# Kernel tuning notes

Measured on AMD Instinct MI355X. Metric: run time of the kernel, lower is better.

## Reference

```python
import jax, jax.numpy as jnp
import numpy as np

B, D, L = 64, 1024, 2048  # batch, init dim, source length; context feature dim = D//2


def setup_inputs() -> dict:
    key = jax.random.key(0)
    k1, k2, k3, k4 = jax.random.split(key, 4)
    inp = jax.random.normal(k1, (B, D), dtype=jnp.float32)
    context = jax.random.normal(k2, (B, L, D // 2), dtype=jnp.float32)
    # torch Linear weights: [out_features, in_features]
    W_in = jax.random.normal(k3, (D, D), dtype=jnp.float32) * (1.0 / np.sqrt(D))
    W_out = jax.random.normal(k4, (D, 2 * D), dtype=jnp.float32) * (1.0 / np.sqrt(2 * D))
    return {"input": inp, "context": context, "W_in": W_in, "W_out": W_out}


def reference(input, context, W_in, W_out):
    Bv, Dv = input.shape
    # linear_in(input).view(B, D//2, 2): two query vectors of size D//2 per batch
    targetT = (input @ W_in.T).reshape(Bv, Dv // 2, 2)           # [B, D/2, 2]
    attn = jnp.einsum('bld,bdk->bkl', context, targetT)          # [B, 2, L]
    attn = jax.nn.softmax(attn, axis=-1)                         # softmax over sourceL
    weighted = jnp.einsum('bkl,bld->bkd', attn, context)         # [B, 2, D/2]
    weightedContext = weighted.reshape(Bv, Dv)                   # [B, D]
    combined = jnp.concatenate([weightedContext, input], axis=1) # [B, 2D]
    contextOutput = jnp.tanh(combined @ W_out.T)                 # [B, D]
    return contextOutput, attn[:, 0, :], attn[:, 1, :]
```

## Files before the change

kernel.cpp:

```cpp
#include <hip/hip_runtime.h>
#include <cmath>

#define NB 64
#define ND 1024
#define DH 512
#define NL 2048
#define NCHUNK 16
#define RPB 128
#define RPW 32
#define REC 520

__global__ __launch_bounds__(256) void k_gemm(const float* __restrict__ A,
                                              const float* __restrict__ W,
                                              float* __restrict__ out,
                                              int K, int do_tanh) {
  __shared__ float As[64][65];
  __shared__ float Ws[4][65];
  const int t = threadIdx.x;
  const int jt = blockIdx.x * 4;
  const int b = t & 63, jl = t >> 6;
  float acc = 0.f;
  for (int m0 = 0; m0 < K; m0 += 64) {
#pragma unroll
    for (int i = 0; i < 4; i++) {
      int f = t + i * 256;
      int r = f >> 4, c = (f & 15) * 4;
      const float4 v = *(const float4*)(A + (size_t)r * K + m0 + c);
      As[r][c] = v.x; As[r][c + 1] = v.y; As[r][c + 2] = v.z; As[r][c + 3] = v.w;
    }
    if (t < 64) {
      int r = t >> 4, c = (t & 15) * 4;
      const float4 v = *(const float4*)(W + (size_t)(jt + r) * K + m0 + c);
      Ws[r][c] = v.x; Ws[r][c + 1] = v.y; Ws[r][c + 2] = v.z; Ws[r][c + 3] = v.w;
    }
    __syncthreads();
#pragma unroll
    for (int mm = 0; mm < 64; mm++) acc += As[b][mm] * Ws[jl][mm];
    __syncthreads();
  }
  out[(size_t)b * ND + jt + jl] = do_tanh ? tanhf(acc) : acc;
}

__global__ __launch_bounds__(256, 4) void k2_attn(const float* __restrict__ ctx,
                                                  const float* __restrict__ tgt,
                                                  float* __restrict__ sc0,
                                                  float* __restrict__ sc1,
                                                  float* __restrict__ part) {
  const int chunk = blockIdx.x, b = blockIdx.y;
  const int wave = threadIdx.x >> 6, lane = threadIdx.x & 63;
  const float* crow = ctx + ((size_t)b * NL + chunk * RPB + wave * RPW) * DH + lane * 8;

  float t0[8], t1[8];
  {
    const float* tp = tgt + b * ND + lane * 16;
#pragma unroll
    for (int j = 0; j < 4; j++) {
      float4 v = *(const float4*)(tp + j * 4);
      t0[2 * j] = v.x; t1[2 * j] = v.y; t0[2 * j + 1] = v.z; t1[2 * j + 1] = v.w;
    }
  }

  float m0 = -INFINITY, l0 = 0.f, m1 = -INFINITY, l1 = 0.f;
  float a0[8], a1[8];
#pragma unroll
  for (int j = 0; j < 8; j++) { a0[j] = 0.f; a1[j] = 0.f; }
  float sv0 = 0.f, sv1 = 0.f;

  float4 pa = *(const float4*)(crow);
  float4 pb = *(const float4*)(crow + 4);
#pragma unroll 2
  for (int i = 0; i < RPW; i++) {
    float c[8] = {pa.x, pa.y, pa.z, pa.w, pb.x, pb.y, pb.z, pb.w};
    if (i + 1 < RPW) {
      pa = *(const float4*)(crow + (size_t)(i + 1) * DH);
      pb = *(const float4*)(crow + (size_t)(i + 1) * DH + 4);
    }
    float s0 = 0.f, s1 = 0.f;
#pragma unroll
    for (int j = 0; j < 8; j++) { s0 += c[j] * t0[j]; s1 += c[j] * t1[j]; }
#pragma unroll
    for (int off = 32; off > 0; off >>= 1) {
      s0 += __shfl_xor(s0, off);
      s1 += __shfl_xor(s1, off);
    }
    if (lane == i) { sv0 = s0; sv1 = s1; }
    if (s0 > m0) {
      float al = __expf(m0 - s0);
      m0 = s0; l0 *= al;
#pragma unroll
      for (int j = 0; j < 8; j++) a0[j] *= al;
    }
    {
      float p = __expf(s0 - m0);
      l0 += p;
#pragma unroll
      for (int j = 0; j < 8; j++) a0[j] += p * c[j];
    }
    if (s1 > m1) {
      float al = __expf(m1 - s1);
      m1 = s1; l1 *= al;
#pragma unroll
      for (int j = 0; j < 8; j++) a1[j] *= al;
    }
    {
      float p = __expf(s1 - m1);
      l1 += p;
#pragma unroll
      for (int j = 0; j < 8; j++) a1[j] += p * c[j];
    }
  }

  const int rowbase = b * NL + chunk * RPB + wave * RPW;
  if (lane < RPW) { sc0[rowbase + lane] = sv0; sc1[rowbase + lane] = sv1; }

  __shared__ float accS[4][1024];
  __shared__ float mlS[4][4];
#pragma unroll
  for (int j = 0; j < 8; j++) {
    accS[wave][lane * 8 + j] = a0[j];
    accS[wave][512 + lane * 8 + j] = a1[j];
  }
  if (lane == 0) { mlS[wave][0] = m0; mlS[wave][1] = l0; mlS[wave][2] = m1; mlS[wave][3] = l1; }
  __syncthreads();

  const int t = threadIdx.x;
  const int k = (t * 4) >> 9;
  const int d = (t * 4) & 511;
  float M = fmaxf(fmaxf(mlS[0][2 * k], mlS[1][2 * k]), fmaxf(mlS[2][2 * k], mlS[3][2 * k]));
  float Lk = 0.f;
  float v0 = 0.f, v1 = 0.f, v2 = 0.f, v3 = 0.f;
#pragma unroll
  for (int w = 0; w < 4; w++) {
    float e = __expf(mlS[w][2 * k] - M);
    Lk += mlS[w][2 * k + 1] * e;
    const float* ap = &accS[w][k * 512 + d];
    v0 += ap[0] * e; v1 += ap[1] * e; v2 += ap[2] * e; v3 += ap[3] * e;
  }
  float* rec = part + ((size_t)(b * NCHUNK + chunk) * 2 + k) * REC;
  if ((t & 127) == 0) { rec[0] = M; rec[1] = Lk; }
  rec[4 + d] = v0; rec[5 + d] = v1; rec[6 + d] = v2; rec[7 + d] = v3;
}

__global__ __launch_bounds__(256) void k3_combine(const float* __restrict__ part,
                                                  const float* __restrict__ inp,
                                                  float* __restrict__ combined,
                                                  float* __restrict__ sc0,
                                                  float* __restrict__ sc1) {
  const int b = blockIdx.x;
  const int t = threadIdx.x;
  __shared__ float MM[2], LL[2];
  if (t < 2) {
    const int k = t;
    float Mk = -INFINITY;
    for (int c = 0; c < NCHUNK; c++)
      Mk = fmaxf(Mk, part[((size_t)(b * NCHUNK + c) * 2 + k) * REC]);
    float Lk = 0.f;
    for (int c = 0; c < NCHUNK; c++) {
      const float* rec = part + ((size_t)(b * NCHUNK + c) * 2 + k) * REC;
      Lk += rec[1] * __expf(rec[0] - Mk);
    }
    MM[k] = Mk; LL[k] = Lk;
  }
  __syncthreads();

  const int k = (t * 4) >> 9, d = (t * 4) & 511;
  float v0 = 0.f, v1 = 0.f, v2 = 0.f, v3 = 0.f;
  for (int c = 0; c < NCHUNK; c++) {
    const float* rec = part + ((size_t)(b * NCHUNK + c) * 2 + k) * REC;
    float e = __expf(rec[0] - MM[k]);
    v0 += rec[4 + d] * e; v1 += rec[5 + d] * e; v2 += rec[6 + d] * e; v3 += rec[7 + d] * e;
  }
  const float inv = 1.f / LL[k];
  float* cp = combined + (size_t)b * 2048 + k * 512 + d;
  cp[0] = v0 * inv; cp[1] = v1 * inv; cp[2] = v2 * inv; cp[3] = v3 * inv;

  const float4 iv = *(const float4*)(inp + (size_t)b * ND + t * 4);
  *(float4*)(combined + (size_t)b * 2048 + 1024 + t * 4) = iv;

  const float M0 = MM[0], i0 = 1.f / LL[0];
  const float M1 = MM[1], i1 = 1.f / LL[1];
#pragma unroll
  for (int r = 0; r < 8; r++) {
    const int idx = b * NL + t * 8 + r;
    sc0[idx] = __expf(sc0[idx] - M0) * i0;
    sc1[idx] = __expf(sc1[idx] - M1) * i1;
  }
}

extern "C" void kernel_launch(void* const* d_in, const int* in_sizes, int n_in,
                              void* d_out, int out_size, void* d_ws, size_t ws_size,
                              hipStream_t stream) {
  const float* input   = (const float*)d_in[0];
  const float* context = (const float*)d_in[1];
  const float* W_in    = (const float*)d_in[2];
  const float* W_out   = (const float*)d_in[3];

  float* out   = (float*)d_out;
  float* attn0 = out + NB * ND;
  float* attn1 = attn0 + NB * NL;

  float* ws       = (float*)d_ws;
  float* target   = ws;
  float* combined = ws + NB * ND;
  float* part     = ws + NB * ND + NB * 2048;

  k_gemm<<<dim3(ND / 4), dim3(256), 0, stream>>>(input, W_in, target, ND, 0);
  k2_attn<<<dim3(NCHUNK, NB), dim3(256), 0, stream>>>(context, target, attn0, attn1, part);
  k3_combine<<<dim3(NB), dim3(256), 0, stream>>>(part, input, combined, attn0, attn1);
  k_gemm<<<dim3(ND / 4), dim3(256), 0, stream>>>(combined, W_out, out, 2 * ND, 1);
}
```

Measured before the change: 451.5 us.

## Split-K GEMMs with register-tiled weights and two-row batched online softmax

Both GEMMs are restructured into split-K kernels. Each wave computes 8 output columns for all 64 batch rows, reading weights directly from global memory as float4 and staging only the activation slab in shared memory; a separate reduce kernel sums the 8 partials and applies tanh where needed. The attention kernel now handles two context rows per iteration, so the online-softmax rescale and exp run once per row pair with a deeper register prefetch. The cost is two extra launches and a partial-sum buffer in workspace, traded against better weight reuse and less serial dependency in the softmax loop.

```diff
diff --git a/kernel.cpp b/kernel.cpp
--- a/kernel.cpp
+++ b/kernel.cpp
@@ -9,36 +9,66 @@
 #define RPB 128
 #define RPW 32
 #define REC 520
-
+#define KS 8
+
+template <int KK>
 __global__ __launch_bounds__(256) void k_gemm(const float* __restrict__ A,
                                               const float* __restrict__ W,
-                                              float* __restrict__ out,
-                                              int K, int do_tanh) {
-  __shared__ float As[64][65];
-  __shared__ float Ws[4][65];
+                                              float* __restrict__ part) {
+  constexpr int SLAB = KK / KS;
+  __shared__ float As[64][36];
   const int t = threadIdx.x;
-  const int jt = blockIdx.x * 4;
-  const int b = t & 63, jl = t >> 6;
-  float acc = 0.f;
-  for (int m0 = 0; m0 < K; m0 += 64) {
-#pragma unroll
-    for (int i = 0; i < 4; i++) {
-      int f = t + i * 256;
-      int r = f >> 4, c = (f & 15) * 4;
-      const float4 v = *(const float4*)(A + (size_t)r * K + m0 + c);
-      As[r][c] = v.x; As[r][c + 1] = v.y; As[r][c + 2] = v.z; As[r][c + 3] = v.w;
-    }
-    if (t < 64) {
-      int r = t >> 4, c = (t & 15) * 4;
-      const float4 v = *(const float4*)(W + (size_t)(jt + r) * K + m0 + c);
-      Ws[r][c] = v.x; Ws[r][c + 1] = v.y; Ws[r][c + 2] = v.z; Ws[r][c + 3] = v.w;
-    }
+  const int lane = t & 63;
+  const int wv = t >> 6;
+  const int k0 = blockIdx.y * SLAB;
+  const int j0 = __builtin_amdgcn_readfirstlane((int)(blockIdx.x * 32 + wv * 8));
+  const float* Wb = W + (size_t)j0 * KK + k0;
+
+  float acc[8];
+#pragma unroll
+  for (int j = 0; j < 8; j++) acc[j] = 0.f;
+
+  const int srow = t >> 2, sko = (t & 3) * 8;
+  const float* sbase = A + (size_t)srow * KK + k0 + sko;
+
+  for (int kc = 0; kc < SLAB; kc += 32) {
+    float4 v0 = *(const float4*)(sbase + kc);
+    float4 v1 = *(const float4*)(sbase + kc + 4);
     __syncthreads();
-#pragma unroll
-    for (int mm = 0; mm < 64; mm++) acc += As[b][mm] * Ws[jl][mm];
+    *(float4*)&As[srow][sko]     = v0;
+    *(float4*)&As[srow][sko + 4] = v1;
     __syncthreads();
-  }
-  out[(size_t)b * ND + jt + jl] = do_tanh ? tanhf(acc) : acc;
+#pragma unroll
+    for (int kk = 0; kk < 32; kk += 4) {
+      float4 av = *(const float4*)&As[lane][kk];
+      const float* wp = Wb + kc + kk;
+#pragma unroll
+      for (int j = 0; j < 8; j++) {
+        float4 wq = *(const float4*)(wp + (size_t)j * KK);
+        acc[j] = fmaf(av.x, wq.x, acc[j]);
+        acc[j] = fmaf(av.y, wq.y, acc[j]);
+        acc[j] = fmaf(av.z, wq.z, acc[j]);
+        acc[j] = fmaf(av.w, wq.w, acc[j]);
+      }
+    }
+  }
+  float* p = part + ((size_t)blockIdx.y * 64 + lane) * ND + j0;
+#pragma unroll
+  for (int j = 0; j < 8; j++) p[j] = acc[j];
+}
+
+template <int ACT>
+__global__ __launch_bounds__(256) void k_reduce(const float* __restrict__ part,
+                                                float* __restrict__ out) {
+  const int i = (blockIdx.x * 256 + threadIdx.x) * 4;
+  float4 s = make_float4(0.f, 0.f, 0.f, 0.f);
+#pragma unroll
+  for (int ks = 0; ks < KS; ks++) {
+    float4 v = *(const float4*)(part + (size_t)ks * (64 * ND) + i);
+    s.x += v.x; s.y += v.y; s.z += v.z; s.w += v.w;
+  }
+  if (ACT) { s.x = tanhf(s.x); s.y = tanhf(s.y); s.z = tanhf(s.z); s.w = tanhf(s.w); }
+  *(float4*)(out + i) = s;
 }
 
 __global__ __launch_bounds__(256, 4) void k2_attn(const float* __restrict__ ctx,
@@ -66,48 +96,64 @@
   for (int j = 0; j < 8; j++) { a0[j] = 0.f; a1[j] = 0.f; }
   float sv0 = 0.f, sv1 = 0.f;
 
-  float4 pa = *(const float4*)(crow);
-  float4 pb = *(const float4*)(crow + 4);
+  float4 cur[4], nxt[4];
+  cur[0] = *(const float4*)(crow);
+  cur[1] = *(const float4*)(crow + 4);
+  cur[2] = *(const float4*)(crow + DH);
+  cur[3] = *(const float4*)(crow + DH + 4);
+
 #pragma unroll 2
-  for (int i = 0; i < RPW; i++) {
-    float c[8] = {pa.x, pa.y, pa.z, pa.w, pb.x, pb.y, pb.z, pb.w};
-    if (i + 1 < RPW) {
-      pa = *(const float4*)(crow + (size_t)(i + 1) * DH);
-      pb = *(const float4*)(crow + (size_t)(i + 1) * DH + 4);
-    }
-    float s0 = 0.f, s1 = 0.f;
-#pragma unroll
-    for (int j = 0; j < 8; j++) { s0 += c[j] * t0[j]; s1 += c[j] * t1[j]; }
-#pragma unroll
-    for (int off = 32; off > 0; off >>= 1) {
-      s0 += __shfl_xor(s0, off);
-      s1 += __shfl_xor(s1, off);
-    }
-    if (lane == i) { sv0 = s0; sv1 = s1; }
-    if (s0 > m0) {
-      float al = __expf(m0 - s0);
-      m0 = s0; l0 *= al;
-#pragma unroll
-      for (int j = 0; j < 8; j++) a0[j] *= al;
-    }
+  for (int ib = 0; ib < 16; ib++) {
+    if (ib < 15) {
+      const float* p = crow + (size_t)(2 * ib + 2) * DH;
+      nxt[0] = *(const float4*)(p);
+      nxt[1] = *(const float4*)(p + 4);
+      nxt[2] = *(const float4*)(p + DH);
+      nxt[3] = *(const float4*)(p + DH + 4);
+    }
+    const float* C = (const float*)cur;
+
+    float s0[2], s1[2];
+#pragma unroll
+    for (int r = 0; r < 2; r++) {
+      float x0 = 0.f, x1 = 0.f;
+#pragma unroll
+      for (int j = 0; j < 8; j++) { x0 += C[r * 8 + j] * t0[j]; x1 += C[r * 8 + j] * t1[j]; }
+      s0[r] = x0; s1[r] = x1;
+    }
+#pragma unroll
+    for (int off = 32; off; off >>= 1) {
+      s0[0] += __shfl_xor(s0[0], off);
+      s0[1] += __shfl_xor(s0[1], off);
+      s1[0] += __shfl_xor(s1[0], off);
+      s1[1] += __shfl_xor(s1[1], off);
+    }
+#pragma unroll
+    for (int r = 0; r < 2; r++)
+      if (lane == 2 * ib + r) { sv0 = s0[r]; sv1 = s1[r]; }
+
     {
-      float p = __expf(s0 - m0);
-      l0 += p;
-#pragma unroll
-      for (int j = 0; j < 8; j++) a0[j] += p * c[j];
-    }
-    if (s1 > m1) {
-      float al = __expf(m1 - s1);
-      m1 = s1; l1 *= al;
-#pragma unroll
-      for (int j = 0; j < 8; j++) a1[j] *= al;
+      float mn = fmaxf(m0, fmaxf(s0[0], s0[1]));
+      float al = __expf(m0 - mn);
+      float p0 = __expf(s0[0] - mn), p1 = __expf(s0[1] - mn);
+      l0 = l0 * al + p0 + p1;
+      m0 = mn;
+#pragma unroll
+      for (int j = 0; j < 8; j++)
+        a0[j] = a0[j] * al + p0 * C[j] + p1 * C[8 + j];
     }
     {
-      float p = __expf(s1 - m1);
-      l1 += p;
-#pragma unroll
-      for (int j = 0; j < 8; j++) a1[j] += p * c[j];
-    }
+      float mn = fmaxf(m1, fmaxf(s1[0], s1[1]));
+      float al = __expf(m1 - mn);
+      float p0 = __expf(s1[0] - mn), p1 = __expf(s1[1] - mn);
+      l1 = l1 * al + p0 + p1;
+      m1 = mn;
+#pragma unroll
+      for (int j = 0; j < 8; j++)
+        a1[j] = a1[j] * al + p0 * C[j] + p1 * C[8 + j];
+    }
+#pragma unroll
+    for (int i = 0; i < 4; i++) cur[i] = nxt[i];
   }
 
   const int rowbase = b * NL + chunk * RPB + wave * RPW;
@@ -201,11 +247,14 @@
 
   float* ws       = (float*)d_ws;
   float* target   = ws;
-  float* combined = ws + NB * ND;
-  float* part     = ws + NB * ND + NB * 2048;
-
-  k_gemm<<<dim3(ND / 4), dim3(256), 0, stream>>>(input, W_in, target, ND, 0);
-  k2_attn<<<dim3(NCHUNK, NB), dim3(256), 0, stream>>>(context, target, attn0, attn1, part);
-  k3_combine<<<dim3(NB), dim3(256), 0, stream>>>(part, input, combined, attn0, attn1);
-  k_gemm<<<dim3(ND / 4), dim3(256), 0, stream>>>(combined, W_out, out, 2 * ND, 1);
-}
+  float* combined = target + NB * ND;
+  float* apart    = combined + NB * 2048;
+  float* gpart    = apart + NB * NCHUNK * 2 * REC;
+
+  k_gemm<ND><<<dim3(32, KS), dim3(256), 0, stream>>>(input, W_in, gpart);
+  k_reduce<0><<<dim3(64), dim3(256), 0, stream>>>(gpart, target);
+  k2_attn<<<dim3(NCHUNK, NB), dim3(256), 0, stream>>>(context, target, attn0, attn1, apart);
+  k3_combine<<<dim3(NB), dim3(256), 0, stream>>>(apart, input, combined, attn0, attn1);
+  k_gemm<2 * ND><<<dim3(32, KS), dim3(256), 0, stream>>>(combined, W_out, gpart);
+  k_reduce<1><<<dim3(64), dim3(256), 0, stream>>>(gpart, out);
+}
```

Result: no change. 451.5 us (-0.0%).
